# Performance work log

Hardware: AMD Instinct MI355X
Metric: run time of the kernel (lower is better)

## Reference

```python
import jax, jax.numpy as jnp
import numpy as np

B, D_IN, D_H, H = 8192, 1024, 1024, 4
HD = D_H // H          # 256 head dim
D_P = int(D_H * 4 / 3) # 1365 projection dim


def setup_inputs() -> dict:
    key = jax.random.key(0)
    ks = jax.random.split(key, 16)
    s = 0.02
    inp = {
        'x': jax.random.normal(ks[0], (B, D_IN), jnp.float32),
        'h_prev': jnp.zeros((B, D_H), jnp.float32),
        'c_prev': jnp.zeros((B, D_H), jnp.float32),
        'n_prev': jnp.zeros((B, D_H), jnp.float32),
        'm_prev': jnp.zeros((B, D_H), jnp.float32),
        'ln_w': jnp.ones((D_IN,), jnp.float32),
        'ln_b': jnp.zeros((D_IN,), jnp.float32),
        'Wz': jax.random.normal(ks[1], (D_IN, D_H)) * s,
        'bz': jnp.zeros((D_H,)),
        'Wi': jax.random.normal(ks[2], (D_IN, D_H)) * s,
        'bi': jnp.zeros((D_H,)),
        'Wf': jax.random.normal(ks[3], (D_IN, D_H)) * s,
        'bf': jnp.zeros((D_H,)),
        'Wo': jax.random.normal(ks[4], (D_IN, D_H)) * s,
        'bo': jnp.zeros((D_H,)),
        'Rz': jax.random.normal(ks[5], (H, HD, HD)) * s,
        'rbz': jnp.zeros((D_H,)),
        'Ri': jax.random.normal(ks[6], (H, HD, HD)) * s,
        'rbi': jnp.zeros((D_H,)),
        'Rf': jax.random.normal(ks[7], (H, HD, HD)) * s,
        'rbf': jnp.zeros((D_H,)),
        'Ro': jax.random.normal(ks[8], (H, HD, HD)) * s,
        'rbo': jnp.zeros((D_H,)),
        'gn_w': jnp.ones((D_H,)),
        'gn_b': jnp.zeros((D_H,)),
        'Wup': jax.random.normal(ks[9], (D_H, 2 * D_P)) * s,
        'bup': jnp.zeros((2 * D_P,)),
        'Wdown': jax.random.normal(ks[10], (D_P, D_IN)) * s,
        'bdown': jnp.zeros((D_IN,)),
    }
    return inp


def reference(x, h_prev, c_prev, n_prev, m_prev,
              ln_w, ln_b,
              Wz, bz, Wi, bi, Wf, bf, Wo, bo,
              Rz, rbz, Ri, rbi, Rf, rbf, Ro, rbo,
              gn_w, gn_b, Wup, bup, Wdown, bdown):
    EPS = 1e-5
    # LayerNorm over input_dim
    mu = x.mean(-1, keepdims=True)
    var = x.var(-1, keepdims=True)
    x_oz = (x - mu) / jnp.sqrt(var + EPS) * ln_w + ln_b
    x_fi = x_oz  # use_conv=False

    # block-diagonal recurrence: per-head (HD x HD) matmul
    hr = h_prev.reshape(B, H, HD)
    def blk(R, rb):
        return jnp.einsum('bhd,hde->bhe', hr, R).reshape(B, D_H) + rb

    z_t = x_oz @ Wz + bz + blk(Rz, rbz)
    i_t = x_fi @ Wi + bi + blk(Ri, rbi)
    f_t = x_fi @ Wf + bf + blk(Rf, rbf)
    o_t = x_fi @ Wo + bo + blk(Ro, rbo)

    zt = jnp.tanh(z_t)
    ot = jax.nn.sigmoid(o_t)
    mt = jnp.maximum(f_t + m_prev, i_t)          # stabilizer
    it = jnp.exp(i_t - mt)
    ft = jnp.exp(f_t + m_prev - mt)
    ct = ft * c_prev + it * zt
    nt = ft * n_prev + it
    ht = ot * (ct / (nt + 1e-13))

    # GroupNorm(num_heads, hidden_dim) on (B, D_H)
    g = ht.reshape(B, H, HD)
    gm = g.mean(-1, keepdims=True)
    gv = g.var(-1, keepdims=True)
    ht_norm = ((g - gm) / jnp.sqrt(gv + EPS)).reshape(B, D_H) * gn_w + gn_b

    # GeGLU feedforward + residual
    up = ht_norm @ Wup + bup
    s_, g_ = up[:, :D_P], up[:, D_P:]
    y = (s_ * jax.nn.gelu(g_, approximate=False)) @ Wdown + bdown + x
    return (y, ht, ct, nt, mt)
```

## Files before the change

### kernel.cpp

```cpp
#include <hip/hip_runtime.h>
#include <hip/hip_bf16.h>
#include <math.h>

#define B_ROWS 8192
#define DIN    1024
#define DH     1024
#define HD     256
#define DP     1365
#define DP2    2730
#define NUP    2816
#define KDN    1408

typedef __bf16 bf16x8 __attribute__((ext_vector_type(8)));
typedef float  f32x4  __attribute__((ext_vector_type(4)));
typedef unsigned short ushort_t;

__device__ __forceinline__ unsigned short f2bf(float f) {
    union { __hip_bfloat16 b; unsigned short u; } v; v.b = __float2bfloat16(f); return v.u;
}
__device__ __forceinline__ float bf2f(unsigned short u) {
    union { __hip_bfloat16 b; unsigned short u; } v; v.u = u; return __bfloat162float(v.b);
}

__global__ __launch_bounds__(256) void prep_hprev(const float* __restrict__ hp,
                                                  ushort_t* __restrict__ out) {
    size_t i = ((size_t)blockIdx.x * 256 + threadIdx.x) * 8;
    float4 a = *(const float4*)(hp + i);
    float4 b = *(const float4*)(hp + i + 4);
    union { unsigned short s[8]; uint4 v; } o;
    o.s[0] = f2bf(a.x); o.s[1] = f2bf(a.y); o.s[2] = f2bf(a.z); o.s[3] = f2bf(a.w);
    o.s[4] = f2bf(b.x); o.s[5] = f2bf(b.y); o.s[6] = f2bf(b.z); o.s[7] = f2bf(b.w);
    *(uint4*)(out + i) = o.v;
}

__global__ __launch_bounds__(256) void prep_wgates(
    const float* __restrict__ Wz, const float* __restrict__ Wi,
    const float* __restrict__ Wf, const float* __restrict__ Wo,
    const float* __restrict__ Rz, const float* __restrict__ Ri,
    const float* __restrict__ Rf, const float* __restrict__ Ro,
    ushort_t* __restrict__ WT) {
    int g = blockIdx.z;
    const float* W = (g == 0) ? Wz : (g == 1) ? Wi : (g == 2) ? Wf : Wo;
    const float* R = (g == 0) ? Rz : (g == 1) ? Ri : (g == 2) ? Rf : Ro;
    int n  = blockIdx.x * 256 + threadIdx.x;
    int k0 = blockIdx.y * 8;
    union { unsigned short s[8]; uint4 v; } o;
    if (k0 < 1024) {
        #pragma unroll
        for (int j = 0; j < 8; ++j) o.s[j] = f2bf(W[(size_t)(k0 + j) * DH + n]);
    } else {
        int h = n >> 8, e = n & 255, d0 = k0 - 1024;
        #pragma unroll
        for (int j = 0; j < 8; ++j) o.s[j] = f2bf(R[h * 65536 + (d0 + j) * 256 + e]);
    }
    *(uint4*)(WT + (size_t)g * 1024 * 1280 + (size_t)n * 1280 + k0) = o.v;
}

__global__ __launch_bounds__(256) void prep_wup(const float* __restrict__ Wup,
                                                ushort_t* __restrict__ WupT) {
    int n  = blockIdx.x * 256 + threadIdx.x;
    int k0 = blockIdx.y * 8;
    union { unsigned short s[8]; uint4 v; } o;
    #pragma unroll
    for (int j = 0; j < 8; ++j)
        o.s[j] = (n < DP2) ? f2bf(Wup[(size_t)(k0 + j) * DP2 + n]) : (unsigned short)0;
    *(uint4*)(WupT + (size_t)n * 1024 + k0) = o.v;
}

__global__ __launch_bounds__(256) void prep_wdown(const float* __restrict__ Wdown,
                                                  ushort_t* __restrict__ WdnT) {
    int n  = blockIdx.x * 256 + threadIdx.x;
    int k0 = blockIdx.y * 8;
    union { unsigned short s[8]; uint4 v; } o;
    #pragma unroll
    for (int j = 0; j < 8; ++j) {
        int k = k0 + j;
        o.s[j] = (k < DP) ? f2bf(Wdown[(size_t)k * DIN + n]) : (unsigned short)0;
    }
    *(uint4*)(WdnT + (size_t)n * KDN + k0) = o.v;
}

__global__ __launch_bounds__(256) void ln_kernel(const float* __restrict__ x,
                                                 const float* __restrict__ w,
                                                 const float* __restrict__ b,
                                                 ushort_t* __restrict__ xn) {
    int row = blockIdx.x;
    int tid = threadIdx.x;
    const float4 v = *(const float4*)(x + (size_t)row * DIN + tid * 4);
    float s  = v.x + v.y + v.z + v.w;
    float sq = v.x*v.x + v.y*v.y + v.z*v.z + v.w*v.w;
    #pragma unroll
    for (int off = 32; off; off >>= 1) {
        s  += __shfl_xor(s, off);
        sq += __shfl_xor(sq, off);
    }
    __shared__ float ss[8];
    int wid = tid >> 6, lane = tid & 63;
    if (lane == 0) { ss[wid] = s; ss[4 + wid] = sq; }
    __syncthreads();
    s  = ss[0] + ss[1] + ss[2] + ss[3];
    sq = ss[4] + ss[5] + ss[6] + ss[7];
    float mu  = s * (1.0f / DIN);
    float var = sq * (1.0f / DIN) - mu * mu;
    float inv = rsqrtf(var + 1e-5f);
    int c = tid * 4;
    float4 wv = *(const float4*)(w + c);
    float4 bv = *(const float4*)(b + c);
    union { unsigned short s4[4]; uint2 v2; } o;
    o.s4[0] = f2bf((v.x - mu) * inv * wv.x + bv.x);
    o.s4[1] = f2bf((v.y - mu) * inv * wv.y + bv.y);
    o.s4[2] = f2bf((v.z - mu) * inv * wv.z + bv.z);
    o.s4[3] = f2bf((v.w - mu) * inv * wv.w + bv.w);
    *(uint2*)(xn + (size_t)row * DIN + c) = o.v2;
}

template<int NK, int SW>
__device__ __forceinline__ void gemm_core256(
    const ushort_t* __restrict__ aP0, const ushort_t* __restrict__ aP1, int lda,
    const ushort_t* __restrict__ bP, int ldb,
    char* AshB, char* BshB, f32x4 (&acc)[8][4])
{
    int tid = threadIdx.x, lane = tid & 63, wave = tid >> 6;
    int wm = wave >> 2, wn = wave & 3;
    int trow = tid >> 1, koff = (tid & 1) * 16;
    int l15 = lane & 15, l4 = lane >> 4;
    int wA  = ((trow >> 4) << 10) + ((tid & 1) << 9) + ((trow & 15) << 4);
    int raA = (wm << 13) + (l4 << 8) + (l15 << 4);
    int raB = (wn << 12) + (l4 << 8) + (l15 << 4);
    const ushort_t* aRow0 = aP0 + (size_t)trow * lda + koff;
    const ushort_t* aRow1 = aP1 + (size_t)trow * lda + koff;
    const ushort_t* bRow  = bP  + (size_t)trow * ldb + koff;

    auto loadAB = [&](int kt, bf16x8& a0, bf16x8& a1, bf16x8& b0, bf16x8& b1) {
        const ushort_t* p = (SW >= NK || kt < SW) ? aRow0 + kt * 32
                                                  : aRow1 + (kt - SW) * 32;
        a0 = *(const bf16x8*)p;
        a1 = *(const bf16x8*)(p + 8);
        const ushort_t* q = bRow + kt * 32;
        b0 = *(const bf16x8*)q;
        b1 = *(const bf16x8*)(q + 8);
    };
    auto stage = [&](char* A, char* B_, bf16x8 a0, bf16x8 a1, bf16x8 b0, bf16x8 b1) {
        *(bf16x8*)(A + wA)        = a0;
        *(bf16x8*)(A + wA + 256)  = a1;
        *(bf16x8*)(B_ + wA)       = b0;
        *(bf16x8*)(B_ + wA + 256) = b1;
    };
    auto compute = [&](const char* A, const char* B_) {
        bf16x8 af[8], bv[4];
        #pragma unroll
        for (int i = 0; i < 8; ++i) af[i] = *(const bf16x8*)(A + raA + i * 1024);
        #pragma unroll
        for (int i = 0; i < 4; ++i) bv[i] = *(const bf16x8*)(B_ + raB + i * 1024);
        #pragma unroll
        for (int mi = 0; mi < 8; ++mi)
            #pragma unroll
            for (int ni = 0; ni < 4; ++ni)
                acc[mi][ni] = __builtin_amdgcn_mfma_f32_16x16x32_bf16(af[mi], bv[ni], acc[mi][ni], 0, 0, 0);
    };

    {
        bf16x8 a0, a1, b0, b1;
        loadAB(0, a0, a1, b0, b1);
        stage(AshB, BshB, a0, a1, b0, b1);
    }
    __syncthreads();
    for (int kt = 0; kt < NK; kt += 2) {
        bf16x8 a0, a1, b0, b1;
        loadAB(kt + 1, a0, a1, b0, b1);
        compute(AshB, BshB);
        stage(AshB + 16384, BshB + 16384, a0, a1, b0, b1);
        __syncthreads();
        if (kt + 2 < NK) loadAB(kt + 2, a0, a1, b0, b1);
        compute(AshB + 16384, BshB + 16384);
        if (kt + 2 < NK) {
            stage(AshB, BshB, a0, a1, b0, b1);
            __syncthreads();
        }
    }
}

__global__ __launch_bounds__(512, 2) void gemm_gates_bf(
    const ushort_t* __restrict__ xn, const ushort_t* __restrict__ hp,
    const ushort_t* __restrict__ WT,
    const float* __restrict__ bz, const float* __restrict__ bi,
    const float* __restrict__ bf_, const float* __restrict__ bo,
    const float* __restrict__ rbz, const float* __restrict__ rbi,
    const float* __restrict__ rbf, const float* __restrict__ rbo,
    ushort_t* __restrict__ gates) {
    int bid = blockIdx.x + (blockIdx.y << 2) + (blockIdx.z << 7);
    int wgs = (bid & 7) * 64 + (bid >> 3);
    int bxi = wgs & 3, rest = wgs >> 2, byi = rest & 31, g = rest >> 5;
    const float* bias = (g == 0) ? bz  : (g == 1) ? bi  : (g == 2) ? bf_ : bo;
    const float* rb   = (g == 0) ? rbz : (g == 1) ? rbi : (g == 2) ? rbf : rbo;
    const ushort_t* Wg = WT + (size_t)g * 1024 * 1280;
    int m0 = byi * 256, n0 = bxi * 256, head = bxi;

    __shared__ __align__(16) char Ash[2][16384];
    __shared__ __align__(16) char Bsh[2][16384];
    f32x4 acc[8][4];
    #pragma unroll
    for (int i = 0; i < 8; ++i)
        #pragma unroll
        for (int j = 0; j < 4; ++j) acc[i][j] = (f32x4){0.f, 0.f, 0.f, 0.f};

    gemm_core256<40, 32>(xn + (size_t)m0 * 1024,
                         hp + (size_t)m0 * 1024 + head * 256, 1024,
                         Wg + (size_t)n0 * 1280, 1280,
                         &Ash[0][0], &Bsh[0][0], acc);

    int lane = threadIdx.x & 63, wave = threadIdx.x >> 6;
    int wm = wave >> 2, wn = wave & 3;
    int l15 = lane & 15, l4 = lane >> 4;
    ushort_t* og = gates + (size_t)g * B_ROWS * DH;
    #pragma unroll
    for (int ni = 0; ni < 4; ++ni) {
        int col = n0 + wn * 64 + ni * 16 + l15;
        float badd = bias[col] + rb[col];
        #pragma unroll
        for (int mi = 0; mi < 8; ++mi) {
            int rbase = m0 + wm * 128 + mi * 16 + l4 * 4;
            #pragma unroll
            for (int j = 0; j < 4; ++j)
                og[(size_t)(rbase + j) * DH + col] = f2bf(acc[mi][ni][j] + badd);
        }
    }
}

__global__ __launch_bounds__(256) void pointwise_gn(
    const ushort_t* __restrict__ gbf,
    const float* __restrict__ c_prev, const float* __restrict__ n_prev,
    const float* __restrict__ m_prev, const float* __restrict__ gn_w,
    const float* __restrict__ gn_b, float* __restrict__ out,
    ushort_t* __restrict__ htn) {
    int row = blockIdx.x;
    int tid = threadIdx.x;
    int head = tid >> 6, lane = tid & 63;
    int col = head * HD + lane * 4;
    size_t idx = (size_t)row * DH + col;
    const size_t N = (size_t)B_ROWS * DH;

    float zv[4], ivv[4], fv[4], ov[4];
    {
        union { uint2 v; unsigned short s[4]; } t;
        t.v = *(const uint2*)(gbf + idx);
        for (int j = 0; j < 4; ++j) zv[j] = bf2f(t.s[j]);
        t.v = *(const uint2*)(gbf + N + idx);
        for (int j = 0; j < 4; ++j) ivv[j] = bf2f(t.s[j]);
        t.v = *(const uint2*)(gbf + 2 * N + idx);
        for (int j = 0; j < 4; ++j) fv[j] = bf2f(t.s[j]);
        t.v = *(const uint2*)(gbf + 3 * N + idx);
        for (int j = 0; j < 4; ++j) ov[j] = bf2f(t.s[j]);
    }
    float4 cp = *(const float4*)(c_prev + idx);
    float4 np = *(const float4*)(n_prev + idx);
    float4 mp = *(const float4*)(m_prev + idx);
    float cpv[4] = {cp.x, cp.y, cp.z, cp.w};
    float npv[4] = {np.x, np.y, np.z, np.w};
    float mpv[4] = {mp.x, mp.y, mp.z, mp.w};

    float htv[4], ctv[4], ntv[4], mtv[4];
    float s = 0.f, sq = 0.f;
    #pragma unroll
    for (int j = 0; j < 4; ++j) {
        float zt = tanhf(zv[j]);
        float ot = 1.0f / (1.0f + expf(-ov[j]));
        float mt = fmaxf(fv[j] + mpv[j], ivv[j]);
        float it = expf(ivv[j] - mt);
        float ft = expf(fv[j] + mpv[j] - mt);
        float ct = ft * cpv[j] + it * zt;
        float nt = ft * npv[j] + it;
        float h  = ot * (ct / (nt + 1e-13f));
        htv[j] = h; ctv[j] = ct; ntv[j] = nt; mtv[j] = mt;
        s += h; sq += h * h;
    }
    *(float4*)(out + N     + idx) = make_float4(htv[0], htv[1], htv[2], htv[3]);
    *(float4*)(out + 2 * N + idx) = make_float4(ctv[0], ctv[1], ctv[2], ctv[3]);
    *(float4*)(out + 3 * N + idx) = make_float4(ntv[0], ntv[1], ntv[2], ntv[3]);
    *(float4*)(out + 4 * N + idx) = make_float4(mtv[0], mtv[1], mtv[2], mtv[3]);

    #pragma unroll
    for (int off = 1; off < 64; off <<= 1) {
        s  += __shfl_xor(s, off);
        sq += __shfl_xor(sq, off);
    }
    float mean = s * (1.0f / HD);
    float var  = fmaxf(sq * (1.0f / HD) - mean * mean, 0.0f);
    float inv  = rsqrtf(var + 1e-5f);
    float4 gw = *(const float4*)(gn_w + col);
    float4 gb = *(const float4*)(gn_b + col);
    float gwv[4] = {gw.x, gw.y, gw.z, gw.w};
    float gbv[4] = {gb.x, gb.y, gb.z, gb.w};
    union { unsigned short s4[4]; uint2 v2; } o;
    #pragma unroll
    for (int j = 0; j < 4; ++j)
        o.s4[j] = f2bf((htv[j] - mean) * inv * gwv[j] + gbv[j]);
    *(uint2*)(htn + idx) = o.v2;
}

__global__ __launch_bounds__(512, 2) void gemm_up_bf(const ushort_t* __restrict__ htn,
                                                     const ushort_t* __restrict__ WupT,
                                                     const float* __restrict__ bup,
                                                     ushort_t* __restrict__ up) {
    int bid = blockIdx.x + blockIdx.y * 11;
    int wgs = (bid & 7) * 44 + (bid >> 3);
    int bxi = wgs % 11, byi = wgs / 11;
    int m0 = byi * 256, n0 = bxi * 256;

    __shared__ __align__(16) char Ash[2][16384];
    __shared__ __align__(16) char Bsh[2][16384];
    f32x4 acc[8][4];
    #pragma unroll
    for (int i = 0; i < 8; ++i)
        #pragma unroll
        for (int j = 0; j < 4; ++j) acc[i][j] = (f32x4){0.f, 0.f, 0.f, 0.f};

    const ushort_t* aP = htn + (size_t)m0 * 1024;
    gemm_core256<32, 32>(aP, aP, 1024, WupT + (size_t)n0 * 1024, 1024,
                         &Ash[0][0], &Bsh[0][0], acc);

    int lane = threadIdx.x & 63, wave = threadIdx.x >> 6;
    int wm = wave >> 2, wn = wave & 3;
    int l15 = lane & 15, l4 = lane >> 4;
    #pragma unroll
    for (int ni = 0; ni < 4; ++ni) {
        int col = n0 + wn * 64 + ni * 16 + l15;
        float badd = (col < DP2) ? bup[col] : 0.f;
        #pragma unroll
        for (int mi = 0; mi < 8; ++mi) {
            int rbase = m0 + wm * 128 + mi * 16 + l4 * 4;
            #pragma unroll
            for (int j = 0; j < 4; ++j)
                up[(size_t)(rbase + j) * NUP + col] = f2bf(acc[mi][ni][j] + badd);
        }
    }
}

__global__ __launch_bounds__(256) void gelu_kernel(const ushort_t* __restrict__ up,
                                                   ushort_t* __restrict__ act) {
    int row = blockIdx.y;
    int c = blockIdx.x * 256 + threadIdx.x;
    if (c >= KDN) return;
    float v = 0.f;
    if (c < DP) {
        float s = bf2f(up[(size_t)row * NUP + c]);
        float g = bf2f(up[(size_t)row * NUP + DP + c]);
        v = s * 0.5f * g * (1.0f + erff(g * 0.70710678118654752f));
    }
    act[(size_t)row * KDN + c] = f2bf(v);
}

__global__ __launch_bounds__(512, 2) void gemm_down_bf(const ushort_t* __restrict__ act,
                                                       const ushort_t* __restrict__ WdnT,
                                                       const float* __restrict__ bdown,
                                                       const float* __restrict__ x,
                                                       float* __restrict__ y) {
    int bid = blockIdx.x + (blockIdx.y << 2);
    int wgs = (bid & 7) * 16 + (bid >> 3);
    int bxi = wgs & 3, byi = wgs >> 2;
    int m0 = byi * 256, n0 = bxi * 256;

    __shared__ __align__(16) char Ash[2][16384];
    __shared__ __align__(16) char Bsh[2][16384];
    f32x4 acc[8][4];
    #pragma unroll
    for (int i = 0; i < 8; ++i)
        #pragma unroll
        for (int j = 0; j < 4; ++j) acc[i][j] = (f32x4){0.f, 0.f, 0.f, 0.f};

    const ushort_t* aP = act + (size_t)m0 * KDN;
    gemm_core256<44, 44>(aP, aP, KDN, WdnT + (size_t)n0 * KDN, KDN,
                         &Ash[0][0], &Bsh[0][0], acc);

    int lane = threadIdx.x & 63, wave = threadIdx.x >> 6;
    int wm = wave >> 2, wn = wave & 3;
    int l15 = lane & 15, l4 = lane >> 4;
    #pragma unroll
    for (int ni = 0; ni < 4; ++ni) {
        int col = n0 + wn * 64 + ni * 16 + l15;
        float bd = bdown[col];
        #pragma unroll
        for (int mi = 0; mi < 8; ++mi) {
            int rbase = m0 + wm * 128 + mi * 16 + l4 * 4;
            #pragma unroll
            for (int j = 0; j < 4; ++j) {
                int r = rbase + j;
                y[(size_t)r * DIN + col] = acc[mi][ni][j] + bd + x[(size_t)r * DIN + col];
            }
        }
    }
}

extern "C" void kernel_launch(void* const* d_in, const int* in_sizes, int n_in,
                              void* d_out, int out_size, void* d_ws, size_t ws_size,
                              hipStream_t stream) {
    (void)in_sizes; (void)n_in; (void)out_size; (void)ws_size;
    const float* x      = (const float*)d_in[0];
    const float* h_prev = (const float*)d_in[1];
    const float* c_prev = (const float*)d_in[2];
    const float* n_prev = (const float*)d_in[3];
    const float* m_prev = (const float*)d_in[4];
    const float* ln_w   = (const float*)d_in[5];
    const float* ln_b   = (const float*)d_in[6];
    const float* Wz = (const float*)d_in[7];  const float* bz = (const float*)d_in[8];
    const float* Wi = (const float*)d_in[9];  const float* bi = (const float*)d_in[10];
    const float* Wf = (const float*)d_in[11]; const float* bf_ = (const float*)d_in[12];
    const float* Wo = (const float*)d_in[13]; const float* bo = (const float*)d_in[14];
    const float* Rz = (const float*)d_in[15]; const float* rbz = (const float*)d_in[16];
    const float* Ri = (const float*)d_in[17]; const float* rbi = (const float*)d_in[18];
    const float* Rf = (const float*)d_in[19]; const float* rbf = (const float*)d_in[20];
    const float* Ro = (const float*)d_in[21]; const float* rbo = (const float*)d_in[22];
    const float* gn_w = (const float*)d_in[23]; const float* gn_b = (const float*)d_in[24];
    const float* Wup  = (const float*)d_in[25]; const float* bup  = (const float*)d_in[26];
    const float* Wdown = (const float*)d_in[27]; const float* bdown = (const float*)d_in[28];

    char* w = (char*)d_ws;
    ushort_t* hp_bf  = (ushort_t*)(w);
    ushort_t* WTg    = (ushort_t*)(w + 16777216);
    ushort_t* WupT   = (ushort_t*)(w + 27262976);
    ushort_t* WdnT   = (ushort_t*)(w + 33030144);
    ushort_t* xn_bf  = (ushort_t*)(w + 35913728);
    ushort_t* htn_bf = xn_bf;
    char*     big    = w + 52690944;
    ushort_t* gates_bf = (ushort_t*)big;
    ushort_t* up_bf    = (ushort_t*)big;
    ushort_t* act_bf   = (ushort_t*)(big + 46137344);
    float* out = (float*)d_out;

    prep_hprev <<<4096, 256, 0, stream>>>(h_prev, hp_bf);
    prep_wgates<<<dim3(4, 160, 4), 256, 0, stream>>>(Wz, Wi, Wf, Wo, Rz, Ri, Rf, Ro, WTg);
    prep_wup   <<<dim3(11, 128), 256, 0, stream>>>(Wup, WupT);
    prep_wdown <<<dim3(4, 176), 256, 0, stream>>>(Wdown, WdnT);
    ln_kernel  <<<B_ROWS, 256, 0, stream>>>(x, ln_w, ln_b, xn_bf);

    gemm_gates_bf<<<dim3(4, 32, 4), 512, 0, stream>>>(
        xn_bf, hp_bf, WTg, bz, bi, bf_, bo, rbz, rbi, rbf, rbo, gates_bf);

    pointwise_gn<<<B_ROWS, 256, 0, stream>>>(
        gates_bf, c_prev, n_prev, m_prev, gn_w, gn_b, out, htn_bf);

    gemm_up_bf<<<dim3(11, 32), 512, 0, stream>>>(htn_bf, WupT, bup, up_bf);

    gelu_kernel<<<dim3(6, B_ROWS), 256, 0, stream>>>(up_bf, act_bf);

    gemm_down_bf<<<dim3(4, 32), 512, 0, stream>>>(act_bf, WdnT, bdown, x, out);
}
```

Measured before the change: 678.8 us.

## Use async global-to-LDS GEMM loads, fuse GeGLU into up-GEMM, retile down-GEMM

Replaces the register-staged GEMM core with direct global_load_lds transfers, explicit vmcnt waits, barriers and s_setprio around the MFMA blocks. Interleaves the Wup columns so each up-GEMM tile holds matching value and gate columns, which lets GeGLU run in the epilogue and removes the separate gelu kernel and its intermediate buffer. Retiles the down GEMM to 256x128 tiles so more workgroups launch. The hand-written waitcnt and barrier sequence must match the number of loads in flight exactly, and any mismatch risks races.

After: 715.8 us. 1.05x slower.

```diff
diff --git a/kernel.cpp b/kernel.cpp
--- a/kernel.cpp
+++ b/kernel.cpp
@@ -8,7 +8,6 @@
 #define HD     256
 #define DP     1365
 #define DP2    2730
-#define NUP    2816
 #define KDN    1408
 
 typedef __bf16 bf16x8 __attribute__((ext_vector_type(8)));
@@ -20,6 +19,10 @@
 }
 __device__ __forceinline__ float bf2f(unsigned short u) {
     union { __hip_bfloat16 b; unsigned short u; } v; v.u = u; return __bfloat162float(v.b);
+}
+__device__ __forceinline__ void gl16(const ushort_t* g, char* l) {
+    __builtin_amdgcn_global_load_lds((const __attribute__((address_space(1))) void*)g,
+                                     (__attribute__((address_space(3))) void*)l, 16, 0, 0);
 }
 
 __global__ __launch_bounds__(256) void prep_hprev(const float* __restrict__ hp,
@@ -60,10 +63,14 @@
                                                 ushort_t* __restrict__ WupT) {
     int n  = blockIdx.x * 256 + threadIdx.x;
     int k0 = blockIdx.y * 8;
+    int t = n >> 8, off = n & 255, q = (off >> 6) & 3, r = off & 63;
+    int oc  = t * 128 + q * 32 + (r & 31);
+    int col = (r < 32) ? oc : DP + oc;
+    bool valid = oc < DP;
     union { unsigned short s[8]; uint4 v; } o;
     #pragma unroll
     for (int j = 0; j < 8; ++j)
-        o.s[j] = (n < DP2) ? f2bf(Wup[(size_t)(k0 + j) * DP2 + n]) : (unsigned short)0;
+        o.s[j] = valid ? f2bf(Wup[(size_t)(k0 + j) * DP2 + col]) : (unsigned short)0;
     *(uint4*)(WupT + (size_t)n * 1024 + k0) = o.v;
 }
 
@@ -114,69 +121,72 @@
     *(uint2*)(xn + (size_t)row * DIN + c) = o.v2;
 }
 
-template<int NK, int SW>
-__device__ __forceinline__ void gemm_core256(
+template<int NB, int MI, int NKT, int SW>
+__device__ __forceinline__ void gemm_async(
     const ushort_t* __restrict__ aP0, const ushort_t* __restrict__ aP1, int lda,
     const ushort_t* __restrict__ bP, int ldb,
-    char* AshB, char* BshB, f32x4 (&acc)[8][4])
+    char* __restrict__ L0, char* __restrict__ L1,
+    f32x4 (&acc)[MI][4])
 {
-    int tid = threadIdx.x, lane = tid & 63, wave = tid >> 6;
-    int wm = wave >> 2, wn = wave & 3;
-    int trow = tid >> 1, koff = (tid & 1) * 16;
-    int l15 = lane & 15, l4 = lane >> 4;
-    int wA  = ((trow >> 4) << 10) + ((tid & 1) << 9) + ((trow & 15) << 4);
-    int raA = (wm << 13) + (l4 << 8) + (l15 << 4);
-    int raB = (wn << 12) + (l4 << 8) + (l15 << 4);
-    const ushort_t* aRow0 = aP0 + (size_t)trow * lda + koff;
-    const ushort_t* aRow1 = aP1 + (size_t)trow * lda + koff;
-    const ushort_t* bRow  = bP  + (size_t)trow * ldb + koff;
-
-    auto loadAB = [&](int kt, bf16x8& a0, bf16x8& a1, bf16x8& b0, bf16x8& b1) {
-        const ushort_t* p = (SW >= NK || kt < SW) ? aRow0 + kt * 32
-                                                  : aRow1 + (kt - SW) * 32;
-        a0 = *(const bf16x8*)p;
-        a1 = *(const bf16x8*)(p + 8);
-        const ushort_t* q = bRow + kt * 32;
-        b0 = *(const bf16x8*)q;
-        b1 = *(const bf16x8*)(q + 8);
+    constexpr int ABYTES = 16384;
+    const int tid = threadIdx.x, lane = tid & 63, wave = tid >> 6;
+    const int wm = wave / NB, wn = wave % NB;
+    const int l15 = lane & 15, l4 = lane >> 4;
+
+    const size_t aOff0 = (size_t)(wave * 32 + l15) * lda + l4 * 8;
+    const size_t aOff1 = aOff0 + (size_t)16 * lda;
+    const size_t bOff0 = (size_t)(wave * (NB * 8) + l15) * ldb + l4 * 8;
+    const size_t bOff1 = bOff0 + (size_t)16 * ldb;
+
+    auto stage = [&](char* L, int kt) {
+        const ushort_t* aT = (SW >= NKT || kt < SW) ? aP0 + kt * 32 : aP1 + (kt - SW) * 32;
+        const ushort_t* bT = bP + kt * 32;
+        gl16(aT + aOff0, L + wave * 2048);
+        gl16(aT + aOff1, L + wave * 2048 + 1024);
+        if constexpr (NB == 4) {
+            gl16(bT + bOff0, L + ABYTES + wave * 2048);
+            gl16(bT + bOff1, L + ABYTES + wave * 2048 + 1024);
+        } else {
+            gl16(bT + bOff0, L + ABYTES + wave * 1024);
+        }
     };
-    auto stage = [&](char* A, char* B_, bf16x8 a0, bf16x8 a1, bf16x8 b0, bf16x8 b1) {
-        *(bf16x8*)(A + wA)        = a0;
-        *(bf16x8*)(A + wA + 256)  = a1;
-        *(bf16x8*)(B_ + wA)       = b0;
-        *(bf16x8*)(B_ + wA + 256) = b1;
-    };
-    auto compute = [&](const char* A, const char* B_) {
-        bf16x8 af[8], bv[4];
-        #pragma unroll
-        for (int i = 0; i < 8; ++i) af[i] = *(const bf16x8*)(A + raA + i * 1024);
-        #pragma unroll
-        for (int i = 0; i < 4; ++i) bv[i] = *(const bf16x8*)(B_ + raB + i * 1024);
-        #pragma unroll
-        for (int mi = 0; mi < 8; ++mi)
+    auto compute = [&](const char* L) {
+        bf16x8 af[MI], bv[4];
+        #pragma unroll
+        for (int mi = 0; mi < MI; ++mi)
+            af[mi] = *(const bf16x8*)(L + (wm * MI + mi) * 1024 + l4 * 256 + l15 * 16);
+        #pragma unroll
+        for (int ni = 0; ni < 4; ++ni)
+            bv[ni] = *(const bf16x8*)(L + ABYTES + (wn * 4 + ni) * 1024 + l4 * 256 + l15 * 16);
+        __builtin_amdgcn_s_setprio(1);
+        #pragma unroll
+        for (int mi = 0; mi < MI; ++mi)
             #pragma unroll
             for (int ni = 0; ni < 4; ++ni)
                 acc[mi][ni] = __builtin_amdgcn_mfma_f32_16x16x32_bf16(af[mi], bv[ni], acc[mi][ni], 0, 0, 0);
+        __builtin_amdgcn_s_setprio(0);
     };
 
-    {
-        bf16x8 a0, a1, b0, b1;
-        loadAB(0, a0, a1, b0, b1);
-        stage(AshB, BshB, a0, a1, b0, b1);
-    }
-    __syncthreads();
-    for (int kt = 0; kt < NK; kt += 2) {
-        bf16x8 a0, a1, b0, b1;
-        loadAB(kt + 1, a0, a1, b0, b1);
-        compute(AshB, BshB);
-        stage(AshB + 16384, BshB + 16384, a0, a1, b0, b1);
-        __syncthreads();
-        if (kt + 2 < NK) loadAB(kt + 2, a0, a1, b0, b1);
-        compute(AshB + 16384, BshB + 16384);
-        if (kt + 2 < NK) {
-            stage(AshB, BshB, a0, a1, b0, b1);
-            __syncthreads();
+    stage(L0, 0);
+    asm volatile("s_waitcnt vmcnt(0)" ::: "memory");
+    asm volatile("s_barrier" ::: "memory");
+    for (int kt = 0; kt < NKT; kt += 2) {
+        stage(L1, kt + 1);
+        if constexpr (NB == 4) asm volatile("s_waitcnt vmcnt(4)" ::: "memory");
+        else                   asm volatile("s_waitcnt vmcnt(3)" ::: "memory");
+        asm volatile("s_barrier" ::: "memory");
+        compute(L0);
+        asm volatile("s_barrier" ::: "memory");
+        if (kt + 2 < NKT) {
+            stage(L0, kt + 2);
+            if constexpr (NB == 4) asm volatile("s_waitcnt vmcnt(4)" ::: "memory");
+            else                   asm volatile("s_waitcnt vmcnt(3)" ::: "memory");
+        } else {
+            asm volatile("s_waitcnt vmcnt(0)" ::: "memory");
         }
+        asm volatile("s_barrier" ::: "memory");
+        compute(L1);
+        asm volatile("s_barrier" ::: "memory");
     }
 }
 
@@ -196,18 +206,17 @@
     const ushort_t* Wg = WT + (size_t)g * 1024 * 1280;
     int m0 = byi * 256, n0 = bxi * 256, head = bxi;
 
-    __shared__ __align__(16) char Ash[2][16384];
-    __shared__ __align__(16) char Bsh[2][16384];
+    __shared__ __align__(16) char L0[32768];
+    __shared__ __align__(16) char L1[32768];
     f32x4 acc[8][4];
     #pragma unroll
     for (int i = 0; i < 8; ++i)
         #pragma unroll
         for (int j = 0; j < 4; ++j) acc[i][j] = (f32x4){0.f, 0.f, 0.f, 0.f};
 
-    gemm_core256<40, 32>(xn + (size_t)m0 * 1024,
-                         hp + (size_t)m0 * 1024 + head * 256, 1024,
-                         Wg + (size_t)n0 * 1280, 1280,
-                         &Ash[0][0], &Bsh[0][0], acc);
+    gemm_async<4, 8, 40, 32>(xn + (size_t)m0 * 1024,
+                             hp + (size_t)m0 * 1024 + head * 256, 1024,
+                             Wg + (size_t)n0 * 1280, 1280, L0, L1, acc);
 
     int lane = threadIdx.x & 63, wave = threadIdx.x >> 6;
     int wm = wave >> 2, wn = wave & 3;
@@ -301,14 +310,14 @@
 __global__ __launch_bounds__(512, 2) void gemm_up_bf(const ushort_t* __restrict__ htn,
                                                      const ushort_t* __restrict__ WupT,
                                                      const float* __restrict__ bup,
-                                                     ushort_t* __restrict__ up) {
+                                                     ushort_t* __restrict__ act) {
     int bid = blockIdx.x + blockIdx.y * 11;
     int wgs = (bid & 7) * 44 + (bid >> 3);
     int bxi = wgs % 11, byi = wgs / 11;
     int m0 = byi * 256, n0 = bxi * 256;
 
-    __shared__ __align__(16) char Ash[2][16384];
-    __shared__ __align__(16) char Bsh[2][16384];
+    __shared__ __align__(16) char L0[32768];
+    __shared__ __align__(16) char L1[32768];
     f32x4 acc[8][4];
     #pragma unroll
     for (int i = 0; i < 8; ++i)
@@ -316,38 +325,28 @@
         for (int j = 0; j < 4; ++j) acc[i][j] = (f32x4){0.f, 0.f, 0.f, 0.f};
 
     const ushort_t* aP = htn + (size_t)m0 * 1024;
-    gemm_core256<32, 32>(aP, aP, 1024, WupT + (size_t)n0 * 1024, 1024,
-                         &Ash[0][0], &Bsh[0][0], acc);
+    gemm_async<4, 8, 32, 32>(aP, aP, 1024, WupT + (size_t)n0 * 1024, 1024, L0, L1, acc);
 
     int lane = threadIdx.x & 63, wave = threadIdx.x >> 6;
     int wm = wave >> 2, wn = wave & 3;
     int l15 = lane & 15, l4 = lane >> 4;
     #pragma unroll
-    for (int ni = 0; ni < 4; ++ni) {
-        int col = n0 + wn * 64 + ni * 16 + l15;
-        float badd = (col < DP2) ? bup[col] : 0.f;
+    for (int ni = 0; ni < 2; ++ni) {
+        int c = bxi * 128 + wn * 32 + ni * 16 + l15;
+        float bs = (c < DP) ? bup[c] : 0.f;
+        float bg = (c < DP) ? bup[DP + c] : 0.f;
         #pragma unroll
         for (int mi = 0; mi < 8; ++mi) {
             int rbase = m0 + wm * 128 + mi * 16 + l4 * 4;
             #pragma unroll
-            for (int j = 0; j < 4; ++j)
-                up[(size_t)(rbase + j) * NUP + col] = f2bf(acc[mi][ni][j] + badd);
+            for (int j = 0; j < 4; ++j) {
+                float sv = acc[mi][ni][j] + bs;
+                float gv = acc[mi][ni + 2][j] + bg;
+                float a  = sv * 0.5f * gv * (1.0f + erff(gv * 0.70710678118654752f));
+                act[(size_t)(rbase + j) * KDN + c] = f2bf(a);
+            }
         }
     }
-}
-
-__global__ __launch_bounds__(256) void gelu_kernel(const ushort_t* __restrict__ up,
-                                                   ushort_t* __restrict__ act) {
-    int row = blockIdx.y;
-    int c = blockIdx.x * 256 + threadIdx.x;
-    if (c >= KDN) return;
-    float v = 0.f;
-    if (c < DP) {
-        float s = bf2f(up[(size_t)row * NUP + c]);
-        float g = bf2f(up[(size_t)row * NUP + DP + c]);
-        v = s * 0.5f * g * (1.0f + erff(g * 0.70710678118654752f));
-    }
-    act[(size_t)row * KDN + c] = f2bf(v);
 }
 
 __global__ __launch_bounds__(512, 2) void gemm_down_bf(const ushort_t* __restrict__ act,
@@ -355,33 +354,32 @@
                                                        const float* __restrict__ bdown,
                                                        const float* __restrict__ x,
                                                        float* __restrict__ y) {
-    int bid = blockIdx.x + (blockIdx.y << 2);
-    int wgs = (bid & 7) * 16 + (bid >> 3);
-    int bxi = wgs & 3, byi = wgs >> 2;
-    int m0 = byi * 256, n0 = bxi * 256;
-
-    __shared__ __align__(16) char Ash[2][16384];
-    __shared__ __align__(16) char Bsh[2][16384];
-    f32x4 acc[8][4];
-    #pragma unroll
-    for (int i = 0; i < 8; ++i)
+    int bid = blockIdx.x + (blockIdx.y << 3);
+    int wgs = (bid & 7) * 32 + (bid >> 3);
+    int bxi = wgs & 7, byi = wgs >> 3;
+    int m0 = byi * 256, n0 = bxi * 128;
+
+    __shared__ __align__(16) char L0[24576];
+    __shared__ __align__(16) char L1[24576];
+    f32x4 acc[4][4];
+    #pragma unroll
+    for (int i = 0; i < 4; ++i)
         #pragma unroll
         for (int j = 0; j < 4; ++j) acc[i][j] = (f32x4){0.f, 0.f, 0.f, 0.f};
 
     const ushort_t* aP = act + (size_t)m0 * KDN;
-    gemm_core256<44, 44>(aP, aP, KDN, WdnT + (size_t)n0 * KDN, KDN,
-                         &Ash[0][0], &Bsh[0][0], acc);
+    gemm_async<2, 4, 44, 44>(aP, aP, KDN, WdnT + (size_t)n0 * KDN, KDN, L0, L1, acc);
 
     int lane = threadIdx.x & 63, wave = threadIdx.x >> 6;
-    int wm = wave >> 2, wn = wave & 3;
+    int wm = wave >> 1, wn = wave & 1;
     int l15 = lane & 15, l4 = lane >> 4;
     #pragma unroll
     for (int ni = 0; ni < 4; ++ni) {
         int col = n0 + wn * 64 + ni * 16 + l15;
         float bd = bdown[col];
         #pragma unroll
-        for (int mi = 0; mi < 8; ++mi) {
-            int rbase = m0 + wm * 128 + mi * 16 + l4 * 4;
+        for (int mi = 0; mi < 4; ++mi) {
+            int rbase = m0 + wm * 64 + mi * 16 + l4 * 4;
             #pragma unroll
             for (int j = 0; j < 4; ++j) {
                 int r = rbase + j;
@@ -423,8 +421,7 @@
     ushort_t* htn_bf = xn_bf;
     char*     big    = w + 52690944;
     ushort_t* gates_bf = (ushort_t*)big;
-    ushort_t* up_bf    = (ushort_t*)big;
-    ushort_t* act_bf   = (ushort_t*)(big + 46137344);
+    ushort_t* act_bf   = (ushort_t*)big;
     float* out = (float*)d_out;
 
     prep_hprev <<<4096, 256, 0, stream>>>(h_prev, hp_bf);
@@ -439,9 +436,7 @@
     pointwise_gn<<<B_ROWS, 256, 0, stream>>>(
         gates_bf, c_prev, n_prev, m_prev, gn_w, gn_b, out, htn_bf);
 
-    gemm_up_bf<<<dim3(11, 32), 512, 0, stream>>>(htn_bf, WupT, bup, up_bf);
-
-    gelu_kernel<<<dim3(6, B_ROWS), 256, 0, stream>>>(up_bf, act_bf);
-
-    gemm_down_bf<<<dim3(4, 32), 512, 0, stream>>>(act_bf, WdnT, bdown, x, out);
-}
+    gemm_up_bf<<<dim3(11, 32), 512, 0, stream>>>(htn_bf, WupT, bup, act_bf);
+
+    gemm_down_bf<<<dim3(8, 32), 512, 0, stream>>>(act_bf, WdnT, bdown, x, out);
+}
```
